# Optimization experiments

Hardware: AMD Instinct MI355X
Metric: run time of the kernel (lower is better)

## Reference

```python
import jax, jax.numpy as jnp
import numpy as np

B, N, D = 8, 256, 16   # batch, set size, in_dim
HID = 256              # hidden width (hidden_dims[:-1])
H = 128                # attention feature dim (hidden_dims[-1])
DH = 64                # per-dim feature dim d_h
NH = 4                 # attention heads


def _made_masks():
    in_deg = np.arange(1, D + 1)
    h_deg = (np.arange(HID) % (D - 1)) + 1
    out_deg = np.repeat(in_deg, H)  # per-dim contiguous layout -> reshape(..., D, H)
    m0 = h_deg[None, :] >= in_deg[:, None]
    m1 = h_deg[None, :] >= h_deg[:, None]
    m2 = out_deg[None, :] > h_deg[:, None]
    return jnp.array(m0), jnp.array(m1), jnp.array(m2)


def setup_inputs() -> dict:
    key = jax.random.key(0)
    ks = iter(jax.random.split(key, 40))
    def w(fi, fo):
        return jax.random.normal(next(ks), (fi, fo), jnp.float32) / np.sqrt(fi)
    inp = {"t": jnp.array([0.5], jnp.float32),
           "x": jax.random.normal(next(ks), (B, N, D), jnp.float32)}
    qd = [D, HID, HID, H * D]
    kd = [D, HID, HID, H]
    dd = [DH + 2, HID, HID, H, 1]
    for i in range(3):
        inp[f"q_w{i}"] = w(qd[i], qd[i + 1]); inp[f"q_b{i}"] = jnp.zeros((qd[i + 1],), jnp.float32)
        inp[f"k_w{i}"] = w(kd[i], kd[i + 1]); inp[f"k_b{i}"] = jnp.zeros((kd[i + 1],), jnp.float32)
        inp[f"v_w{i}"] = w(kd[i], kd[i + 1]); inp[f"v_b{i}"] = jnp.zeros((kd[i + 1],), jnp.float32)
    inp["p_w"] = w(H, DH); inp["p_b"] = jnp.zeros((DH,), jnp.float32)
    for i in range(4):
        inp[f"d_w{i}"] = w(dd[i], dd[i + 1]); inp[f"d_b{i}"] = jnp.zeros((dd[i + 1],), jnp.float32)
    inp["q_m0"], inp["q_m1"], inp["q_m2"] = _made_masks()
    return inp


def reference(t, x, q_w0, q_b0, k_w0, k_b0, v_w0, v_b0, q_w1, q_b1, k_w1, k_b1, v_w1, v_b1,
              q_w2, q_b2, k_w2, k_b2, v_w2, v_b2, p_w, p_b,
              d_w0, d_b0, d_w1, d_b1, d_w2, d_b2, d_w3, d_b3, q_m0, q_m1, q_m2):
    # --- exclusive net: MADE query (hollow per dim), MLP key/value, diagonal-masked attention ---
    hq = jax.nn.relu(x @ (q_w0 * q_m0) + q_b0)
    hq = jax.nn.relu(hq @ (q_w1 * q_m1) + q_b1)
    q = (hq @ (q_w2 * q_m2) + q_b2).reshape(B, N, D, H)      # [B,N,D,H]

    def mlp3(z, w0, b0, w1, b1, w2, b2):
        z = jnp.tanh(z @ w0 + b0)
        z = jnp.tanh(z @ w1 + b1)
        return z @ w2 + b2

    k = mlp3(x, k_w0, k_b0, k_w1, k_b1, k_w2, k_b2)          # [B,N,H] (shared across dims)
    v = mlp3(x, v_w0, v_b0, v_w1, v_b1, v_w2, v_b2)          # [B,N,H]

    dh = H // NH
    qh = q.transpose(0, 2, 1, 3).reshape(B, D, N, NH, dh).transpose(0, 1, 3, 2, 4)  # [B,D,NH,N,dh]
    kh = k.reshape(B, N, NH, dh).transpose(0, 2, 1, 3)        # [B,NH,N,dh]
    vh = v.reshape(B, N, NH, dh).transpose(0, 2, 1, 3)

    # einsum avoids materializing the repeat_interleaved key/value (same math)
    scores = jnp.einsum('bdhnc,bhmc->bdhnm', qh, kh) / np.sqrt(dh)
    scores = jnp.where(jnp.eye(N, dtype=bool), -jnp.inf, scores)  # mask self-attention (hollow)
    att = jax.nn.softmax(scores, axis=-1)
    o = jnp.einsum('bdhnm,bhmc->bdhnc', att, vh)              # [B,D,NH,N,dh]
    o = o.transpose(0, 1, 3, 2, 4).reshape(B, D, N, H).transpose(0, 2, 1, 3)  # [B,N,D,H]
    hfeat = o @ p_w + p_b                                     # [B,N,D,DH], hollow wrt x[...,d]

    # --- dimwise net: y_d = MLP([t, x_d, h_d]); exact diagonal Jacobian via jvp on x channel ---
    tb = jnp.broadcast_to(t.reshape(()), (B, N, D, 1)).astype(x.dtype)
    def dimwise(xc):
        z = jnp.concatenate([tb, xc, hfeat], -1)              # [B,N,D,2+DH]
        z = jnp.tanh(z @ d_w0 + d_b0)
        z = jnp.tanh(z @ d_w1 + d_b1)
        z = jnp.tanh(z @ d_w2 + d_b2)
        return (z @ d_w3 + d_b3)[..., 0]                      # [B,N,D]

    y, jac = jax.jvp(dimwise, (x[..., None],), (jnp.ones((B, N, D, 1), x.dtype),))
    return y, jac
```

## Files before the change

### kernel.cpp

```cpp
#include <hip/hip_runtime.h>
#include <hip/hip_bf16.h>

constexpr int kB = 8, kN = 256, kD = 16, kHID = 256, kH = 128, kDH = 64, kdh = 32;
constexpr int kBN = kB * kN;
constexpr int kP  = kBN * kD;

__device__ __forceinline__ float b2f(__hip_bfloat16 v) { return __bfloat162float(v); }
__device__ __forceinline__ __hip_bfloat16 f2b(float v) { return __float2bfloat16(v); }
__device__ __forceinline__ unsigned short f2bs(float v) {
    __hip_bfloat16 h = __float2bfloat16(v);
    return *(unsigned short*)&h;
}
__device__ __forceinline__ float bs2f(unsigned short s) {
    unsigned int u = ((unsigned int)s) << 16;
    return *(float*)&u;
}

__device__ __forceinline__ float tanh_fast(float v) {
    float e = __expf(2.f * v);
    return 1.f - 2.f * __builtin_amdgcn_rcpf(e + 1.f);
}

typedef short s8v  __attribute__((ext_vector_type(8)));
typedef float f4v  __attribute__((ext_vector_type(4)));
#define MFMA(a, b, c) __builtin_amdgcn_mfma_f32_16x16x32_bf16((a), (b), (c), 0, 0, 0)

__global__ __launch_bounds__(256) void prep_frag(
    const float* p_w, const float* d_w0, const float* d_w1, const float* d_w2,
    const float* k_w0, const float* k_w1, const float* k_w2,
    const float* v_w0, const float* v_w1, const float* v_w2,
    const float* q_w0, const float* q_w1, const float* q_w2,
    __hip_bfloat16* pwf, __hip_bfloat16* w0f, __hip_bfloat16* w1f, __hip_bfloat16* w2f,
    __hip_bfloat16* k0f, __hip_bfloat16* k1f, __hip_bfloat16* k2f,
    __hip_bfloat16* v0f, __hip_bfloat16* v1f, __hip_bfloat16* v2f,
    __hip_bfloat16* q0f, __hip_bfloat16* q1f, __hip_bfloat16* q2f)
{
    const int tile = blockIdx.x * 4 + (threadIdx.x >> 6);
    const int lane = threadIdx.x & 63;
    const float* src; __hip_bfloat16* dst; int N, NT, local, Kreal = 1 << 30, mask = 0;
    if (tile < 16)        { src = p_w;        dst = pwf; N = 64;   NT = 4;   local = tile; }
    else if (tile < 48)   { src = d_w0 + 512; dst = w0f; N = 256;  NT = 16;  local = tile - 16; }
    else if (tile < 176)  { src = d_w1;       dst = w1f; N = 256;  NT = 16;  local = tile - 48; }
    else if (tile < 240)  { src = d_w2;       dst = w2f; N = 128;  NT = 8;   local = tile - 176; }
    else if (tile < 256)  { src = k_w0;       dst = k0f; N = 256;  NT = 16;  local = tile - 240; Kreal = 16; }
    else if (tile < 272)  { src = v_w0;       dst = v0f; N = 256;  NT = 16;  local = tile - 256; Kreal = 16; }
    else if (tile < 288)  { src = q_w0;       dst = q0f; N = 256;  NT = 16;  local = tile - 272; Kreal = 16; mask = 1; }
    else if (tile < 416)  { src = k_w1;       dst = k1f; N = 256;  NT = 16;  local = tile - 288; }
    else if (tile < 544)  { src = v_w1;       dst = v1f; N = 256;  NT = 16;  local = tile - 416; }
    else if (tile < 672)  { src = q_w1;       dst = q1f; N = 256;  NT = 16;  local = tile - 544; mask = 2; }
    else if (tile < 736)  { src = k_w2;       dst = k2f; N = 128;  NT = 8;   local = tile - 672; }
    else if (tile < 800)  { src = v_w2;       dst = v2f; N = 128;  NT = 8;   local = tile - 736; }
    else                  { src = q_w2;       dst = q2f; N = 2048; NT = 128; local = tile - 800; mask = 3; }
    const int kt = local / NT, nt = local % NT;
    const int row0 = kt * 32 + (lane >> 4) * 8;
    const int col  = nt * 16 + (lane & 15);
    __hip_bfloat16* o = dst + ((size_t)local * 64 + lane) * 8;
    #pragma unroll
    for (int j = 0; j < 8; ++j) {
        const int r = row0 + j;
        float w = (r < Kreal) ? src[(size_t)r * N + col] : 0.f;
        if (mask == 1 && !((col % 15) >= r))        w = 0.f;
        if (mask == 2 && !((col % 15) >= (r % 15))) w = 0.f;
        if (mask == 3 && !((col >> 7) > (r % 15)))  w = 0.f;
        o[j] = f2b(w);
    }
}

__global__ __launch_bounds__(256) void mlp_kernel(
    const float* x,
    const float* k_b0, const float* k_b1, const float* k_b2,
    const float* v_b0, const float* v_b1, const float* v_b2,
    const float* q_b0, const float* q_b1,
    const __hip_bfloat16* k0f, const __hip_bfloat16* k1f, const __hip_bfloat16* k2f,
    const __hip_bfloat16* v0f, const __hip_bfloat16* v1f, const __hip_bfloat16* v2f,
    const __hip_bfloat16* q0f, const __hip_bfloat16* q1f,
    __hip_bfloat16* kbuf, __hip_bfloat16* vbuf, __hip_bfloat16* h1q)
{
    constexpr int SA = 264;
    constexpr int SX = 40;
    __shared__ __hip_bfloat16 xin[32 * SX];
    __shared__ __hip_bfloat16 bufA[32 * SA];
    __shared__ __hip_bfloat16 bufB[32 * SA];

    const int tid  = threadIdx.x;
    const int wv   = tid >> 6, lane = tid & 63;
    const int lx   = lane & 15, quad = lane >> 4;
    const int r0   = blockIdx.x * 32;

    auto ldA = [&](const __hip_bfloat16* buf, int stride, int m0, int k0) -> s8v {
        return *(const s8v*)(buf + (m0 + lx) * stride + k0 + quad * 8);
    };
    auto ldB = [&](const __hip_bfloat16* wf, int NT, int kt, int nt) -> s8v {
        return *(const s8v*)(wf + (((size_t)(kt * NT + nt) * 64 + lane) << 3));
    };

    for (int idx = tid; idx < 1024; idx += 256) {
        const int row = idx >> 5, c = idx & 31;
        xin[row * SX + c] = f2b(c < 16 ? x[(r0 + row) * kD + c] : 0.f);
    }

    const __hip_bfloat16* F0[3] = { k0f, v0f, q0f };
    const __hip_bfloat16* F1[3] = { k1f, v1f, q1f };
    const __hip_bfloat16* F2[2] = { k2f, v2f };
    const float* Ba0[3] = { k_b0, v_b0, q_b0 };
    const float* Ba1[3] = { k_b1, v_b1, q_b1 };
    const float* Ba2[2] = { k_b2, v_b2 };
    __hip_bfloat16* O2[2] = { kbuf, vbuf };

    for (int path = 0; path < 3; ++path) {
        __syncthreads();

        {
            f4v acc[4][2] = {};
            const s8v a0 = ldA(xin, SX, 0, 0);
            const s8v a1 = ldA(xin, SX, 16, 0);
            #pragma unroll
            for (int j = 0; j < 4; ++j) {
                s8v b = ldB(F0[path], 16, 0, wv * 4 + j);
                acc[j][0] = MFMA(a0, b, acc[j][0]);
                acc[j][1] = MFMA(a1, b, acc[j][1]);
            }
            #pragma unroll
            for (int j = 0; j < 4; ++j) {
                const int n = (wv * 4 + j) * 16 + lx;
                const float bb = Ba0[path][n];
                #pragma unroll
                for (int mt = 0; mt < 2; ++mt)
                #pragma unroll
                for (int r = 0; r < 4; ++r) {
                    const float v = acc[j][mt][r] + bb;
                    const float z = (path == 2) ? fmaxf(v, 0.f) : tanh_fast(v);
                    bufA[(mt * 16 + quad * 4 + r) * SA + n] = f2b(z);
                }
            }
        }
        __syncthreads();

        {
            f4v acc[4][2] = {};
            #pragma unroll
            for (int kt = 0; kt < 8; ++kt) {
                const s8v a0 = ldA(bufA, SA, 0, kt * 32);
                const s8v a1 = ldA(bufA, SA, 16, kt * 32);
                #pragma unroll
                for (int j = 0; j < 4; ++j) {
                    s8v b = ldB(F1[path], 16, kt, wv * 4 + j);
                    acc[j][0] = MFMA(a0, b, acc[j][0]);
                    acc[j][1] = MFMA(a1, b, acc[j][1]);
                }
            }
            #pragma unroll
            for (int j = 0; j < 4; ++j) {
                const int n = (wv * 4 + j) * 16 + lx;
                const float bb = Ba1[path][n];
                #pragma unroll
                for (int mt = 0; mt < 2; ++mt)
                #pragma unroll
                for (int r = 0; r < 4; ++r) {
                    const int m = mt * 16 + quad * 4 + r;
                    const float v = acc[j][mt][r] + bb;
                    if (path == 2) {
                        h1q[(size_t)(r0 + m) * 256 + n] = f2b(fmaxf(v, 0.f));
                    } else {
                        bufB[m * SA + n] = f2b(tanh_fast(v));
                    }
                }
            }
        }
        if (path == 2) break;
        __syncthreads();

        {
            f4v acc[2][2] = {};
            #pragma unroll
            for (int kt = 0; kt < 8; ++kt) {
                const s8v a0 = ldA(bufB, SA, 0, kt * 32);
                const s8v a1 = ldA(bufB, SA, 16, kt * 32);
                #pragma unroll
                for (int j = 0; j < 2; ++j) {
                    s8v b = ldB(F2[path], 8, kt, wv * 2 + j);
                    acc[j][0] = MFMA(a0, b, acc[j][0]);
                    acc[j][1] = MFMA(a1, b, acc[j][1]);
                }
            }
            #pragma unroll
            for (int j = 0; j < 2; ++j) {
                const int n = (wv * 2 + j) * 16 + lx;
                const float bb = Ba2[path][n];
                #pragma unroll
                for (int mt = 0; mt < 2; ++mt)
                #pragma unroll
                for (int r = 0; r < 4; ++r) {
                    const int m = mt * 16 + quad * 4 + r;
                    O2[path][(size_t)(r0 + m) * kH + n] = f2b(acc[j][mt][r] + bb);
                }
            }
        }
    }
}

__global__ __launch_bounds__(256) void qgemm_kernel(
    const float* q_b2, const __hip_bfloat16* h1q, const __hip_bfloat16* q2f,
    __hip_bfloat16* qbuf)
{
    constexpr int SA = 264;
    __shared__ __hip_bfloat16 hin[32 * SA];

    const int tid  = threadIdx.x;
    const int wv   = tid >> 6, lane = tid & 63;
    const int lx   = lane & 15, quad = lane >> 4;
    const int ct   = blockIdx.x & 7;
    const int r0   = (blockIdx.x >> 3) * 32;

    for (int idx = tid; idx < 1024; idx += 256) {
        const int row = idx >> 5, seg = idx & 31;
        *(f4v*)(hin + row * SA + seg * 8) = *(const f4v*)(h1q + (size_t)(r0 + row) * 256 + seg * 8);
    }
    __syncthreads();

    f4v acc[4][2] = {};
    #pragma unroll
    for (int kt = 0; kt < 8; ++kt) {
        const s8v a0 = *(const s8v*)(hin + lx * SA + kt * 32 + quad * 8);
        const s8v a1 = *(const s8v*)(hin + (16 + lx) * SA + kt * 32 + quad * 8);
        #pragma unroll
        for (int j = 0; j < 4; ++j) {
            s8v b = *(const s8v*)(q2f + (((size_t)(kt * 128 + ct * 16 + wv * 4 + j) * 64 + lane) << 3));
            acc[j][0] = MFMA(a0, b, acc[j][0]);
            acc[j][1] = MFMA(a1, b, acc[j][1]);
        }
    }
    #pragma unroll
    for (int j = 0; j < 4; ++j) {
        const int col = ct * 256 + (wv * 4 + j) * 16 + lx;
        const float bb = q_b2[col];
        #pragma unroll
        for (int mt = 0; mt < 2; ++mt)
        #pragma unroll
        for (int r = 0; r < 4; ++r) {
            const int row = r0 + mt * 16 + quad * 4 + r;
            qbuf[(size_t)row * 2048 + col] = f2b(acc[j][mt][r] + bb);
        }
    }
}

__global__ __launch_bounds__(64, 2) void attn_kernel(
    const __hip_bfloat16* qbuf, const __hip_bfloat16* kbuf, const __hip_bfloat16* vbuf,
    __hip_bfloat16* obuf)
{
    constexpr int SP = 264;
    __shared__ short Pl[16 * SP];

    const int blk = blockIdx.x;
    const int qw = blk & 3;
    const int hd = (blk >> 2) & 3;
    const int d  = (blk >> 4) & 15;
    const int b  = blk >> 8;

    const int lane = threadIdx.x;
    const int lx = lane & 15, quad = lane >> 4;

    const short* kb = (const short*)kbuf;
    const short* vb = (const short*)vbuf;
    const short* qb = (const short*)qbuf;

    s8v kfrag[16];
    #pragma unroll
    for (int mt = 0; mt < 16; ++mt)
        kfrag[mt] = *(const s8v*)(kb + (size_t)(b * 256 + mt * 16 + lx) * 128 + hd * 32 + quad * 8);

    s8v vfrag[2][8];
    #pragma unroll
    for (int ntv = 0; ntv < 2; ++ntv)
    #pragma unroll
    for (int kt = 0; kt < 8; ++kt) {
        s8v v;
        #pragma unroll
        for (int j = 0; j < 8; ++j)
            v[j] = vb[(size_t)(b * 256 + kt * 32 + quad * 8 + j) * 128 + hd * 32 + ntv * 16 + lx];
        vfrag[ntv][kt] = v;
    }

    const float scale = 0.17677669529663687f;

    for (int mi = 0; mi < 4; ++mi) {
        const int q0 = qw * 64 + mi * 16;

        s8v qfrag = *(const s8v*)(qb + (size_t)(b * 256 + q0 + lx) * 2048 + d * 128 + hd * 32 + quad * 8);

        f4v acc[16];
        #pragma unroll
        for (int mt = 0; mt < 16; ++mt) acc[mt] = f4v{0.f, 0.f, 0.f, 0.f};
        #pragma unroll
        for (int mt = 0; mt < 16; ++mt) acc[mt] = MFMA(kfrag[mt], qfrag, acc[mt]);

        const int qg = q0 + lx;
        float mx = -3.0e38f;
        #pragma unroll
        for (int mt = 0; mt < 16; ++mt)
        #pragma unroll
        for (int r = 0; r < 4; ++r) {
            const int key = mt * 16 + quad * 4 + r;
            float s = (key == qg) ? -3.0e38f : acc[mt][r];
            acc[mt][r] = s;
            mx = fmaxf(mx, s);
        }
        mx = fmaxf(mx, __shfl_xor(mx, 16, 64));
        mx = fmaxf(mx, __shfl_xor(mx, 32, 64));

        float l = 0.f;
        #pragma unroll
        for (int mt = 0; mt < 16; ++mt)
        #pragma unroll
        for (int r = 0; r < 4; ++r) {
            float p = __expf((acc[mt][r] - mx) * scale);
            acc[mt][r] = p;
            l += p;
        }
        l += __shfl_xor(l, 16, 64);
        l += __shfl_xor(l, 32, 64);

        #pragma unroll
        for (int mt = 0; mt < 16; ++mt) {
            unsigned short h0 = f2bs(acc[mt][0]);
            unsigned short h1 = f2bs(acc[mt][1]);
            unsigned short h2 = f2bs(acc[mt][2]);
            unsigned short h3 = f2bs(acc[mt][3]);
            uint2 w;
            w.x = (unsigned int)h0 | ((unsigned int)h1 << 16);
            w.y = (unsigned int)h2 | ((unsigned int)h3 << 16);
            *(uint2*)(Pl + lx * SP + mt * 16 + quad * 4) = w;
            acc[mt][0] -= bs2f(h0);
            acc[mt][1] -= bs2f(h1);
            acc[mt][2] -= bs2f(h2);
            acc[mt][3] -= bs2f(h3);
        }
        __asm__ volatile("s_waitcnt lgkmcnt(0)" ::: "memory");

        f4v av[2] = { f4v{0.f,0.f,0.f,0.f}, f4v{0.f,0.f,0.f,0.f} };
        #pragma unroll
        for (int kt = 0; kt < 8; ++kt) {
            s8v a = *(const s8v*)(Pl + lx * SP + kt * 32 + quad * 8);
            av[0] = MFMA(a, vfrag[0][kt], av[0]);
            av[1] = MFMA(a, vfrag[1][kt], av[1]);
        }

        __asm__ volatile("s_waitcnt lgkmcnt(0)" ::: "memory");
        #pragma unroll
        for (int mt = 0; mt < 16; ++mt) {
            unsigned short h0 = f2bs(acc[mt][0]);
            unsigned short h1 = f2bs(acc[mt][1]);
            unsigned short h2 = f2bs(acc[mt][2]);
            unsigned short h3 = f2bs(acc[mt][3]);
            uint2 w;
            w.x = (unsigned int)h0 | ((unsigned int)h1 << 16);
            w.y = (unsigned int)h2 | ((unsigned int)h3 << 16);
            *(uint2*)(Pl + lx * SP + mt * 16 + quad * 4) = w;
        }
        __asm__ volatile("s_waitcnt lgkmcnt(0)" ::: "memory");
        #pragma unroll
        for (int kt = 0; kt < 8; ++kt) {
            s8v a = *(const s8v*)(Pl + lx * SP + kt * 32 + quad * 8);
            av[0] = MFMA(a, vfrag[0][kt], av[0]);
            av[1] = MFMA(a, vfrag[1][kt], av[1]);
        }
        __asm__ volatile("s_waitcnt lgkmcnt(0)" ::: "memory");

        #pragma unroll
        for (int r = 0; r < 4; ++r) {
            const float lr = __shfl(l, quad * 4 + r, 64);
            const float inv = __builtin_amdgcn_rcpf(lr);
            const int qrow = q0 + quad * 4 + r;
            #pragma unroll
            for (int ntv = 0; ntv < 2; ++ntv) {
                obuf[((size_t)((b * 256 + qrow) * 16 + d)) * 128 + hd * 32 + ntv * 16 + lx]
                    = f2b(av[ntv][r] * inv);
            }
        }
    }
}

__global__ __launch_bounds__(256) void dim_kernel(
    const float* t, const float* x,
    const float* p_b, const float* d_w0, const float* d_b0,
    const float* d_b1, const float* d_b2, const float* d_w3, const float* d_b3,
    const __hip_bfloat16* pwf, const __hip_bfloat16* w0f,
    const __hip_bfloat16* w1f, const __hip_bfloat16* w2f,
    const __hip_bfloat16* obuf, float* out)
{
    constexpr int SA = 264;
    constexpr int SO = 136;
    constexpr int SH = 72;
    __shared__ __hip_bfloat16 bufA[64 * SA];
    __shared__ __hip_bfloat16 bufB[64 * SA];
    __shared__ float xvs[32];

    const int tid  = threadIdx.x;
    const int wv   = tid >> 6, lane = tid & 63;
    const int lx   = lane & 15, quad = lane >> 4;
    const int p0   = blockIdx.x * 32;
    const float tval = t[0];

    auto ldA = [&](const __hip_bfloat16* buf, int stride, int m0, int k0) -> s8v {
        return *(const s8v*)(buf + (m0 + lx) * stride + k0 + quad * 8);
    };
    auto ldBf = [&](const __hip_bfloat16* wf, int NT, int kt, int nt) -> s8v {
        return *(const s8v*)(wf + (((size_t)(kt * NT + nt) * 64 + lane) << 3));
    };

    for (int idx = tid; idx < 512; idx += 256) {
        const int row = idx >> 4, ch = idx & 15;
        *(f4v*)(bufA + row * SO + ch * 8) = *(const f4v*)(obuf + (size_t)(p0 + row) * kH + ch * 8);
    }
    if (tid < 32) xvs[tid] = x[p0 + tid];
    __syncthreads();

    {
        f4v acc0 = {}, acc1 = {};
        #pragma unroll
        for (int ktile = 0; ktile < 4; ++ktile) {
            s8v b  = ldBf(pwf, 4, ktile, wv);
            s8v a0 = ldA(bufA, SO, 0,  ktile * 32);
            s8v a1 = ldA(bufA, SO, 16, ktile * 32);
            acc0 = MFMA(a0, b, acc0);
            acc1 = MFMA(a1, b, acc1);
        }
        const int n = wv * 16 + lx;
        const float bb = p_b[n];
        #pragma unroll
        for (int r = 0; r < 4; ++r) {
            bufB[(quad * 4 + r) * SH + n]        = f2b(acc0[r] + bb);
            bufB[(16 + quad * 4 + r) * SH + n]   = f2b(acc1[r] + bb);
        }
    }
    __syncthreads();

    {
        f4v acc[4][2] = {};
        #pragma unroll
        for (int ktile = 0; ktile < 2; ++ktile) {
            s8v a0 = ldA(bufB, SH, 0,  ktile * 32);
            s8v a1 = ldA(bufB, SH, 16, ktile * 32);
            #pragma unroll
            for (int j = 0; j < 4; ++j) {
                s8v b = ldBf(w0f, 16, ktile, wv * 4 + j);
                acc[j][0] = MFMA(a0, b, acc[j][0]);
                acc[j][1] = MFMA(a1, b, acc[j][1]);
            }
        }
        #pragma unroll
        for (int j = 0; j < 4; ++j) {
            const int n = (wv * 4 + j) * 16 + lx;
            const float base = d_b0[n] + tval * d_w0[n];
            const float wx   = d_w0[256 + n];
            #pragma unroll
            for (int mt = 0; mt < 2; ++mt)
            #pragma unroll
            for (int r = 0; r < 4; ++r) {
                const int m = mt * 16 + quad * 4 + r;
                const float z = tanh_fast(acc[j][mt][r] + base + xvs[m] * wx);
                bufA[m * SA + n]        = f2b(z);
                bufA[(m + 32) * SA + n] = f2b((1.f - z * z) * wx);
            }
        }
    }
    __syncthreads();

    {
        f4v acc[4][4] = {};
        #pragma unroll
        for (int ktile = 0; ktile < 8; ++ktile) {
            s8v a[4];
            #pragma unroll
            for (int mt = 0; mt < 4; ++mt) a[mt] = ldA(bufA, SA, mt * 16, ktile * 32);
            #pragma unroll
            for (int j = 0; j < 4; ++j) {
                s8v b = ldBf(w1f, 16, ktile, wv * 4 + j);
                #pragma unroll
                for (int mt = 0; mt < 4; ++mt) acc[j][mt] = MFMA(a[mt], b, acc[j][mt]);
            }
        }
        #pragma unroll
        for (int j = 0; j < 4; ++j) {
            const int n = (wv * 4 + j) * 16 + lx;
            const float b1 = d_b1[n];
            #pragma unroll
            for (int mt = 0; mt < 2; ++mt)
            #pragma unroll
            for (int r = 0; r < 4; ++r) {
                const int m = mt * 16 + quad * 4 + r;
                const float z  = tanh_fast(acc[j][mt][r] + b1);
                const float zd = (1.f - z * z) * acc[j][mt + 2][r];
                bufB[m * SA + n]        = f2b(z);
                bufB[(m + 32) * SA + n] = f2b(zd);
            }
        }
    }
    __syncthreads();

    {
        f4v acc[2][4] = {};
        #pragma unroll
        for (int ktile = 0; ktile < 8; ++ktile) {
            s8v a[4];
            #pragma unroll
            for (int mt = 0; mt < 4; ++mt) a[mt] = ldA(bufB, SA, mt * 16, ktile * 32);
            #pragma unroll
            for (int j = 0; j < 2; ++j) {
                s8v b = ldBf(w2f, 8, ktile, wv * 2 + j);
                #pragma unroll
                for (int mt = 0; mt < 4; ++mt) acc[j][mt] = MFMA(a[mt], b, acc[j][mt]);
            }
        }
        #pragma unroll
        for (int j = 0; j < 2; ++j) {
            const int n = (wv * 2 + j) * 16 + lx;
            const float b2 = d_b2[n];
            #pragma unroll
            for (int mt = 0; mt < 2; ++mt)
            #pragma unroll
            for (int r = 0; r < 4; ++r) {
                const int m = mt * 16 + quad * 4 + r;
                const float z  = tanh_fast(acc[j][mt][r] + b2);
                const float zd = (1.f - z * z) * acc[j][mt + 2][r];
                bufA[m * SO + n]        = f2b(z);
                bufA[(m + 32) * SO + n] = f2b(zd);
            }
        }
    }
    __syncthreads();

    {
        const int p = tid >> 3, s = tid & 7;
        float yv = 0.f, jv = 0.f;
        #pragma unroll
        for (int i = 0; i < 16; ++i) {
            const int n = s + i * 8;
            const float w = d_w3[n];
            yv += b2f(bufA[p * SO + n]) * w;
            jv += b2f(bufA[(p + 32) * SO + n]) * w;
        }
        #pragma unroll
        for (int off = 4; off > 0; off >>= 1) {
            yv += __shfl_down(yv, off, 8);
            jv += __shfl_down(jv, off, 8);
        }
        if (s == 0) {
            out[p0 + p]      = yv + d_b3[0];
            out[kP + p0 + p] = jv;
        }
    }
}

extern "C" void kernel_launch(void* const* d_in, const int* in_sizes, int n_in,
                              void* d_out, int out_size, void* d_ws, size_t ws_size,
                              hipStream_t stream)
{
    typedef const float* fp;
    fp t    = (fp)d_in[0];
    fp x    = (fp)d_in[1];
    fp q_w0 = (fp)d_in[2],  q_b0 = (fp)d_in[3];
    fp k_w0 = (fp)d_in[4],  k_b0 = (fp)d_in[5];
    fp v_w0 = (fp)d_in[6],  v_b0 = (fp)d_in[7];
    fp q_w1 = (fp)d_in[8],  q_b1 = (fp)d_in[9];
    fp k_w1 = (fp)d_in[10], k_b1 = (fp)d_in[11];
    fp v_w1 = (fp)d_in[12], v_b1 = (fp)d_in[13];
    fp q_w2 = (fp)d_in[14], q_b2 = (fp)d_in[15];
    fp k_w2 = (fp)d_in[16], k_b2 = (fp)d_in[17];
    fp v_w2 = (fp)d_in[18], v_b2 = (fp)d_in[19];
    fp p_w  = (fp)d_in[20], p_b  = (fp)d_in[21];
    fp d_w0 = (fp)d_in[22], d_b0 = (fp)d_in[23];
    fp d_w1 = (fp)d_in[24], d_b1 = (fp)d_in[25];
    fp d_w2 = (fp)d_in[26], d_b2 = (fp)d_in[27];
    fp d_w3 = (fp)d_in[28], d_b3 = (fp)d_in[29];

    __hip_bfloat16* wsb  = (__hip_bfloat16*)d_ws;
    __hip_bfloat16* kbuf = wsb;
    __hip_bfloat16* vbuf = kbuf + (size_t)kBN * kH;
    __hip_bfloat16* qbuf = vbuf + (size_t)kBN * kH;
    __hip_bfloat16* obuf = qbuf + (size_t)kBN * kD * kH;
    __hip_bfloat16* pwf  = obuf + (size_t)kP * kH;
    __hip_bfloat16* w0f  = pwf + 8192;
    __hip_bfloat16* w1f  = w0f + 16384;
    __hip_bfloat16* w2f  = w1f + 65536;
    __hip_bfloat16* k0f  = w2f + 32768;
    __hip_bfloat16* v0f  = k0f + 8192;
    __hip_bfloat16* q0f  = v0f + 8192;
    __hip_bfloat16* k1f  = q0f + 8192;
    __hip_bfloat16* v1f  = k1f + 65536;
    __hip_bfloat16* q1f  = v1f + 65536;
    __hip_bfloat16* k2f  = q1f + 65536;
    __hip_bfloat16* v2f  = k2f + 32768;
    __hip_bfloat16* q2f  = v2f + 32768;
    __hip_bfloat16* h1q  = q2f + 524288;

    float* out = (float*)d_out;

    prep_frag<<<456, 256, 0, stream>>>(p_w, d_w0, d_w1, d_w2,
        k_w0, k_w1, k_w2, v_w0, v_w1, v_w2, q_w0, q_w1, q_w2,
        pwf, w0f, w1f, w2f, k0f, k1f, k2f, v0f, v1f, v2f, q0f, q1f, q2f);
    mlp_kernel<<<kBN / 32, 256, 0, stream>>>(x,
        k_b0, k_b1, k_b2, v_b0, v_b1, v_b2, q_b0, q_b1,
        k0f, k1f, k2f, v0f, v1f, v2f, q0f, q1f, kbuf, vbuf, h1q);
    qgemm_kernel<<<(kBN / 32) * 8, 256, 0, stream>>>(q_b2, h1q, q2f, qbuf);
    attn_kernel<<<kB * kD * 4 * 4, 64, 0, stream>>>(qbuf, kbuf, vbuf, obuf);
    dim_kernel<<<kP / 32, 256, 0, stream>>>(t, x, p_b, d_w0, d_b0, d_b1, d_b2, d_w3, d_b3,
        pwf, w0f, w1f, w2f, obuf, out);
}
```

Baseline: 218.4 us.

## Drop split-bf16 P·V pass, fold softmax scale into Q, store attention output fp32

Removes the second hi/lo residual P·V MFMA pass in attention, so probabilities go through one bf16 pass. The softmax scale is folded into the Q GEMM epilogue and exp is computed with exp2 and an FMA. Attention blocks now carry four waves (one per query quarter) instead of one wave each, and the attention output buffer becomes fp32, with dim_kernel converting it to bf16 when loading. This cuts MFMA and LDS work in attention, but doubles the obuf write and read traffic and slightly lowers P·V accuracy.

Result: no change. 215.1 us (-1.5%).

```diff
diff --git a/kernel.cpp b/kernel.cpp
--- a/kernel.cpp
+++ b/kernel.cpp
@@ -10,10 +10,6 @@
 __device__ __forceinline__ unsigned short f2bs(float v) {
     __hip_bfloat16 h = __float2bfloat16(v);
     return *(unsigned short*)&h;
-}
-__device__ __forceinline__ float bs2f(unsigned short s) {
-    unsigned int u = ((unsigned int)s) << 16;
-    return *(float*)&u;
 }
 
 __device__ __forceinline__ float tanh_fast(float v) {
@@ -230,6 +226,7 @@
             acc[j][1] = MFMA(a1, b, acc[j][1]);
         }
     }
+    const float scale = 0.17677669529663687f;
     #pragma unroll
     for (int j = 0; j < 4; ++j) {
         const int col = ct * 256 + (wv * 4 + j) * 16 + lx;
@@ -239,26 +236,27 @@
         #pragma unroll
         for (int r = 0; r < 4; ++r) {
             const int row = r0 + mt * 16 + quad * 4 + r;
-            qbuf[(size_t)row * 2048 + col] = f2b(acc[j][mt][r] + bb);
-        }
-    }
-}
-
-__global__ __launch_bounds__(64, 2) void attn_kernel(
+            qbuf[(size_t)row * 2048 + col] = f2b((acc[j][mt][r] + bb) * scale);
+        }
+    }
+}
+
+__global__ __launch_bounds__(256, 2) void attn_kernel(
     const __hip_bfloat16* qbuf, const __hip_bfloat16* kbuf, const __hip_bfloat16* vbuf,
-    __hip_bfloat16* obuf)
+    float* obuf)
 {
     constexpr int SP = 264;
-    __shared__ short Pl[16 * SP];
+    __shared__ short Pl[4][16 * SP];
 
     const int blk = blockIdx.x;
-    const int qw = blk & 3;
-    const int hd = (blk >> 2) & 3;
-    const int d  = (blk >> 4) & 15;
-    const int b  = blk >> 8;
-
-    const int lane = threadIdx.x;
+    const int hd = blk & 3;
+    const int d  = (blk >> 2) & 15;
+    const int b  = blk >> 6;
+
+    const int wv   = threadIdx.x >> 6;
+    const int lane = threadIdx.x & 63;
     const int lx = lane & 15, quad = lane >> 4;
+    short* Pw = &Pl[wv][0];
 
     const short* kb = (const short*)kbuf;
     const short* vb = (const short*)vbuf;
@@ -281,10 +279,10 @@
         vfrag[ntv][kt] = v;
     }
 
-    const float scale = 0.17677669529663687f;
+    const float LOG2E = 1.4426950408889634f;
 
     for (int mi = 0; mi < 4; ++mi) {
-        const int q0 = qw * 64 + mi * 16;
+        const int q0 = wv * 64 + mi * 16;
 
         s8v qfrag = *(const s8v*)(qb + (size_t)(b * 256 + q0 + lx) * 2048 + d * 128 + hd * 32 + quad * 8);
 
@@ -308,12 +306,13 @@
         mx = fmaxf(mx, __shfl_xor(mx, 16, 64));
         mx = fmaxf(mx, __shfl_xor(mx, 32, 64));
 
+        const float nmxc = -mx * LOG2E;
         float l = 0.f;
         #pragma unroll
         for (int mt = 0; mt < 16; ++mt)
         #pragma unroll
         for (int r = 0; r < 4; ++r) {
-            float p = __expf((acc[mt][r] - mx) * scale);
+            float p = exp2f(__builtin_fmaf(acc[mt][r], LOG2E, nmxc));
             acc[mt][r] = p;
             l += p;
         }
@@ -329,38 +328,14 @@
             uint2 w;
             w.x = (unsigned int)h0 | ((unsigned int)h1 << 16);
             w.y = (unsigned int)h2 | ((unsigned int)h3 << 16);
-            *(uint2*)(Pl + lx * SP + mt * 16 + quad * 4) = w;
-            acc[mt][0] -= bs2f(h0);
-            acc[mt][1] -= bs2f(h1);
-            acc[mt][2] -= bs2f(h2);
-            acc[mt][3] -= bs2f(h3);
+            *(uint2*)(Pw + lx * SP + mt * 16 + quad * 4) = w;
         }
         __asm__ volatile("s_waitcnt lgkmcnt(0)" ::: "memory");
 
         f4v av[2] = { f4v{0.f,0.f,0.f,0.f}, f4v{0.f,0.f,0.f,0.f} };
         #pragma unroll
         for (int kt = 0; kt < 8; ++kt) {
-            s8v a = *(const s8v*)(Pl + lx * SP + kt * 32 + quad * 8);
-            av[0] = MFMA(a, vfrag[0][kt], av[0]);
-            av[1] = MFMA(a, vfrag[1][kt], av[1]);
-        }
-
-        __asm__ volatile("s_waitcnt lgkmcnt(0)" ::: "memory");
-        #pragma unroll
-        for (int mt = 0; mt < 16; ++mt) {
-            unsigned short h0 = f2bs(acc[mt][0]);
-            unsigned short h1 = f2bs(acc[mt][1]);
-            unsigned short h2 = f2bs(acc[mt][2]);
-            unsigned short h3 = f2bs(acc[mt][3]);
-            uint2 w;
-            w.x = (unsigned int)h0 | ((unsigned int)h1 << 16);
-            w.y = (unsigned int)h2 | ((unsigned int)h3 << 16);
-            *(uint2*)(Pl + lx * SP + mt * 16 + quad * 4) = w;
-        }
-        __asm__ volatile("s_waitcnt lgkmcnt(0)" ::: "memory");
-        #pragma unroll
-        for (int kt = 0; kt < 8; ++kt) {
-            s8v a = *(const s8v*)(Pl + lx * SP + kt * 32 + quad * 8);
+            s8v a = *(const s8v*)(Pw + lx * SP + kt * 32 + quad * 8);
             av[0] = MFMA(a, vfrag[0][kt], av[0]);
             av[1] = MFMA(a, vfrag[1][kt], av[1]);
         }
@@ -374,7 +349,7 @@
             #pragma unroll
             for (int ntv = 0; ntv < 2; ++ntv) {
                 obuf[((size_t)((b * 256 + qrow) * 16 + d)) * 128 + hd * 32 + ntv * 16 + lx]
-                    = f2b(av[ntv][r] * inv);
+                    = av[ntv][r] * inv;
             }
         }
     }
@@ -386,7 +361,7 @@
     const float* d_b1, const float* d_b2, const float* d_w3, const float* d_b3,
     const __hip_bfloat16* pwf, const __hip_bfloat16* w0f,
     const __hip_bfloat16* w1f, const __hip_bfloat16* w2f,
-    const __hip_bfloat16* obuf, float* out)
+    const float* obuf, float* out)
 {
     constexpr int SA = 264;
     constexpr int SO = 136;
@@ -408,9 +383,11 @@
         return *(const s8v*)(wf + (((size_t)(kt * NT + nt) * 64 + lane) << 3));
     };
 
-    for (int idx = tid; idx < 512; idx += 256) {
-        const int row = idx >> 4, ch = idx & 15;
-        *(f4v*)(bufA + row * SO + ch * 8) = *(const f4v*)(obuf + (size_t)(p0 + row) * kH + ch * 8);
+    for (int idx = tid; idx < 1024; idx += 256) {
+        const int row = idx >> 5, seg = idx & 31;
+        f4v v = *(const f4v*)(obuf + (size_t)(p0 + row) * kH + seg * 4);
+        __hip_bfloat16* dst = bufA + row * SO + seg * 4;
+        dst[0] = f2b(v[0]); dst[1] = f2b(v[1]); dst[2] = f2b(v[2]); dst[3] = f2b(v[3]);
     }
     if (tid < 32) xvs[tid] = x[p0 + tid];
     __syncthreads();
@@ -574,12 +551,12 @@
     fp d_w2 = (fp)d_in[26], d_b2 = (fp)d_in[27];
     fp d_w3 = (fp)d_in[28], d_b3 = (fp)d_in[29];
 
-    __hip_bfloat16* wsb  = (__hip_bfloat16*)d_ws;
+    float* obuf = (float*)d_ws;
+    __hip_bfloat16* wsb  = (__hip_bfloat16*)(obuf + (size_t)kP * kH);
     __hip_bfloat16* kbuf = wsb;
     __hip_bfloat16* vbuf = kbuf + (size_t)kBN * kH;
     __hip_bfloat16* qbuf = vbuf + (size_t)kBN * kH;
-    __hip_bfloat16* obuf = qbuf + (size_t)kBN * kD * kH;
-    __hip_bfloat16* pwf  = obuf + (size_t)kP * kH;
+    __hip_bfloat16* pwf  = qbuf + (size_t)kBN * kD * kH;
     __hip_bfloat16* w0f  = pwf + 8192;
     __hip_bfloat16* w1f  = w0f + 16384;
     __hip_bfloat16* w2f  = w1f + 65536;
@@ -603,7 +580,7 @@
         k_b0, k_b1, k_b2, v_b0, v_b1, v_b2, q_b0, q_b1,
         k0f, k1f, k2f, v0f, v1f, v2f, q0f, q1f, kbuf, vbuf, h1q);
     qgemm_kernel<<<(kBN / 32) * 8, 256, 0, stream>>>(q_b2, h1q, q2f, qbuf);
-    attn_kernel<<<kB * kD * 4 * 4, 64, 0, stream>>>(qbuf, kbuf, vbuf, obuf);
+    attn_kernel<<<kB * kD * 4, 256, 0, stream>>>(qbuf, kbuf, vbuf, obuf);
     dim_kernel<<<kP / 32, 256, 0, stream>>>(t, x, p_b, d_w0, d_b0, d_b1, d_b2, d_w3, d_b3,
         pwf, w0f, w1f, w2f, obuf, out);
 }
```
